# Performance work log

Measured on AMD Instinct MI355X. Metric: run time of the kernel, lower is better.

The kernel has to match this reference:

```python
import jax, jax.numpy as jnp
import numpy as np

# module config (matches init_kwargs)
SLICE_W, SLICE_H = 32, 32
STRIDE, WIDTH_INIT = 8, 8
EMBED_DIM = 512
B, H, W = 64, 32, 4096
PAD = (SLICE_W - WIDTH_INIT) // 2  # 12, width padding with constant value 1.0


def setup_inputs() -> dict:
    key = jax.random.key(0)
    k1, k2, k3, k4, k5 = jax.random.split(key, 5)
    u = lambda k, s: jax.random.uniform(k, s, jnp.float32, -0.08, 0.08)
    return {
        "images": jax.random.normal(k1, (B, 1, H, W), jnp.float32),
        "conv_w": u(k2, (1, 1, 3, 3)),          # Conv2d(1,1,3x3) weight (OIHW)
        "conv_b": u(k3, (1,)),
        "lin_w": u(k4, (SLICE_W * SLICE_H, EMBED_DIM)),  # bridge Linear, stored [in,out]
        "lin_b": u(k5, (EMBED_DIM,)),
    }


def reference(images, conv_w, conv_b, lin_w, lin_b):
    b = images.shape[0]
    # pad width with constant 1 (F.pad(..., 'constant', 1))
    padded = jnp.pad(images, ((0, 0), (0, 0), (0, 0), (PAD, PAD)), constant_values=1.0)
    # vectorized replacement of the python loop over stride positions
    starts = np.arange(0, W - 1, STRIDE)               # [S] static
    S = starts.shape[0]                                # 512
    idx = starts[:, None] + np.arange(SLICE_W)[None, :]  # [S, slice_w]
    sl = padded[:, :, :, idx]                          # [B,1,H,S,slice_w]
    sl = jnp.transpose(sl, (0, 3, 1, 2, 4))            # [B,S,1,H,slice_w]
    x = sl.reshape(b * S, 1, H, SLICE_W)               # pixels
    # embedder: Conv2d(1,1,k=3,pad=1) + ReLU
    y = jax.lax.conv_general_dilated(x, conv_w, (1, 1), ((1, 1), (1, 1)))
    y = jax.nn.relu(y + conv_b[None, :, None, None])
    # bridge: Linear(slice_w*slice_h -> embed_dim)
    flat = y.reshape(b * S, H * SLICE_W)
    out = flat @ lin_w + lin_b
    return out.reshape(b, S, EMBED_DIM)
```

## Files before the change

### kernel.cpp

```cpp
#include <hip/hip_runtime.h>
#include <cstdint>
#include <cstddef>

typedef unsigned short u16;
typedef unsigned int   u32;
typedef __attribute__((ext_vector_type(4))) float  f32x4;
typedef __attribute__((ext_vector_type(8))) __bf16 bf16x8;

#define PSW   1056
#define ASTR  72
#define CFW   4128
#define RPAD  4144

#define WS_BT  0u
#define WS_CF  1048576u
#define WS_AB  (1048576u + 16908288u)
#define WS_NEED (1048576u + 16908288u + 4194304u)

static __device__ __forceinline__ float b2f(u32 u) {
  union { u32 i; float f; } c; c.i = u << 16; return c.f;
}
static __device__ __forceinline__ u16 f2b(float f) {
  union { float f; u32 i; } c; c.f = f;
  return (u16)((c.i + 0x7FFFu + ((c.i >> 16) & 1u)) >> 16);
}

static __device__ __forceinline__ void gl_lds16(const void* g, void* l) {
  __builtin_amdgcn_global_load_lds(
      (__attribute__((address_space(1))) unsigned int*)(void*)g,
      (__attribute__((address_space(3))) unsigned int*)l, 16, 0, 0);
}
static __device__ __forceinline__ void gl_lds4(const void* g, void* l) {
  __builtin_amdgcn_global_load_lds(
      (__attribute__((address_space(1))) unsigned int*)(void*)g,
      (__attribute__((address_space(3))) unsigned int*)l, 4, 0, 0);
}

__global__ __launch_bounds__(256) void transpose_w(const float* __restrict__ lw,
                                                   u16* __restrict__ bt) {
  __shared__ u16 tile[64][65];
  const int t  = threadIdx.x;
  const int c  = t & 63, r0 = t >> 6;
  const int n0 = blockIdx.x * 64;
  const int k0 = blockIdx.y * 64;
#pragma unroll
  for (int rr = 0; rr < 16; ++rr) {
    const int r = r0 * 16 + rr;
    tile[r][c] = f2b(lw[(size_t)(k0 + r) * 512 + n0 + c]);
  }
  __syncthreads();
#pragma unroll
  for (int rr = 0; rr < 16; ++rr) {
    const int r = r0 * 16 + rr;
    bt[(size_t)(n0 + r) * 1024 + k0 + c] = tile[c][r];
  }
}

__global__ __launch_bounds__(256) void prep(
    const float* __restrict__ img, const float* __restrict__ cw,
    const float* __restrict__ cb, u16* __restrict__ cf, u32* __restrict__ ab)
{
  __shared__ __align__(16) float R[3][RPAD];
  const int b = blockIdx.x, h = blockIdx.y, t = threadIdx.x;
  const float* imgb = img + (size_t)b * 32 * 4096;
#pragma unroll
  for (int r = 0; r < 3; ++r) {
    const int hh = h - 1 + r;
    const int live = (hh >= 0 && hh <= 31);
    const float* row = imgb + (ptrdiff_t)hh * 4096;
    for (int k = t; k < 1024; k += 256) {
      f32x4 v = (f32x4)0.0f;
      if (live) v = *(const f32x4*)(row + (k << 2));
      *(f32x4*)(&R[r][12 + (k << 2)]) = v;
    }
    if (t < 12)      R[r][t] = live ? 1.0f : 0.0f;
    else if (t < 24) R[r][4096 + t] = live ? 1.0f : 0.0f;
    else if (t < 48) R[r][4096 + t] = 0.0f;
  }
  __syncthreads();
  float w[9];
#pragma unroll
  for (int q = 0; q < 9; ++q) w[q] = cw[q];
  const float bias = cb[0];
  u16* dst = cf + (size_t)(b * 32 + h) * CFW;
  for (int c = t; c < 258; c += 256) {
    float wf[3][24];
#pragma unroll
    for (int r = 0; r < 3; ++r) {
      const f32x4* Rr = (const f32x4*)&R[r][0];
      f32x4 m = (f32x4)0.0f;
      if (c != 0) m = Rr[4 * c - 1];
      *(f32x4*)&wf[r][0] = m;
#pragma unroll
      for (int u = 1; u < 6; ++u) *(f32x4*)&wf[r][4 * u] = Rr[4 * c - 1 + u];
    }
    float o[16];
#pragma unroll
    for (int j = 0; j < 16; ++j) o[j] = bias;
#pragma unroll
    for (int r = 0; r < 3; ++r) {
      const float w0 = w[r * 3], w1 = w[r * 3 + 1], w2 = w[r * 3 + 2];
#pragma unroll
      for (int j = 0; j < 16; ++j)
        o[j] += w0 * wf[r][j + 3] + w1 * wf[r][j + 4] + w2 * wf[r][j + 5];
    }
    const int xbase = c << 4;
    u32 pk[8];
#pragma unroll
    for (int q = 0; q < 8; ++q) {
      const int x0 = xbase + 2 * q;
      const u32 lo = (x0     < 4120) ? (u32)f2b(fmaxf(o[2 * q],     0.f)) : 0u;
      const u32 hi = (x0 + 1 < 4120) ? (u32)f2b(fmaxf(o[2 * q + 1], 0.f)) : 0u;
      pk[q] = lo | (hi << 16);
    }
    uint4* dp = (uint4*)(dst + xbase);
    dp[0] = make_uint4(pk[0], pk[1], pk[2], pk[3]);
    dp[1] = make_uint4(pk[4], pk[5], pk[6], pk[7]);
  }
  u32* abrow = ab + (size_t)(b * 32 + h) * 512;
#pragma unroll
  for (int ss = 0; ss < 2; ++ss) {
    const int s = t + ss * 256;
    const int X0 = s << 3;
    float o0 = bias, o1 = bias;
#pragma unroll
    for (int r = 0; r < 3; ++r) {
      o0 += w[r * 3 + 1] * R[r][X0]      + w[r * 3 + 2] * R[r][X0 + 1];
      o1 += w[r * 3 + 0] * R[r][X0 + 30] + w[r * 3 + 1] * R[r][X0 + 31];
    }
    abrow[s] = (u32)f2b(fmaxf(o0, 0.f)) | ((u32)f2b(fmaxf(o1, 0.f)) << 16);
  }
}

__global__ __launch_bounds__(256) void gemm_k(
    const u16* __restrict__ cf, const u32* __restrict__ ab,
    const u16* __restrict__ bt, const float* __restrict__ lb,
    float* __restrict__ out)
{
  __shared__ __align__(16) char sm[4224 + 1024 + 16384];
  u16* Ps   = (u16*)sm;
  u32* Ab32 = (u32*)(sm + 4224);
  u16* Bs   = (u16*)(sm + 5248);
  float* Cs = (float*)sm;

  const int t  = threadIdx.x;
  const int nt = blockIdx.x, mt = blockIdx.y;
  const int b  = mt >> 2, s0 = (mt & 3) << 7, n0 = nt << 7;
  const int w  = t >> 6, i = t & 63;
  const int wr = w >> 1, wc = w & 1;
  const int lq = i >> 4, lr = i & 15;

  const int cB = (i & 7) ^ ((i >> 3) & 7);
  const u16* btp = bt + (size_t)(n0 + (w << 5) + (i >> 3)) * 1024 + (cB << 3);
  u16* BsW = Bs + (w << 11);

  const int rP  = (t >= 132) ? 1 : 0;
  const int ccP = t - 132 * rP;
  const u16* cfp  = cf + (size_t)(b * 32 + rP) * CFW + (s0 << 3) + (ccP << 3);
  const u16* cfp2 = cf + (size_t)(b * 32 + 1) * CFW + (s0 << 3) + ((124 + t) << 3);
  u16* PsW = Ps + (w << 9);

  const u32* abp = ab + (size_t)(b * 32 + (t >> 7)) * 512 + s0 + (t & 127);
  u32* AbW = Ab32 + (w << 6);

  f32x4 acc[4][4];
#pragma unroll
  for (int a = 0; a < 4; ++a)
#pragma unroll
    for (int c = 0; c < 4; ++c) acc[a][c] = (f32x4)0.0f;

  for (int kk = 0; kk < 16; ++kk) {
    __syncthreads();
    gl_lds16(btp,              BsW);
    gl_lds16(btp +  8 * 1024,  BsW + 512);
    gl_lds16(btp + 16 * 1024,  BsW + 1024);
    gl_lds16(btp + 24 * 1024,  BsW + 1536);
    gl_lds16(cfp, PsW);
    if (t < 8) gl_lds16(cfp2, Ps + 2048);
    gl_lds4(abp, AbW);
    btp += 64; cfp += 2 * CFW; cfp2 += 2 * CFW; abp += 1024;
    __syncthreads();

#pragma unroll
    for (int kc = 0; kc < 2; ++kc) {
      const int bswz = (((kc << 2) + lq) ^ (lr & 7)) << 3;
      bf16x8 af[4], bfv[4];
#pragma unroll
      for (int im = 0; im < 4; ++im) {
        const int ml = wr * 64 + im * 16 + lr;
        af[im] = __builtin_bit_cast(bf16x8,
            *(const uint4*)(Ps + kc * 1056 + ((ml + lq) << 3)));
        const u32 a32 = Ab32[kc * 128 + ml];
        union { u16 u; __bf16 h; } lo, hi;
        lo.u = (u16)(a32 & 0xffffu); hi.u = (u16)(a32 >> 16);
        if (lq == 0) af[im][0] = lo.h;
        if (lq == 3) af[im][7] = hi.h;
      }
#pragma unroll
      for (int jn = 0; jn < 4; ++jn) {
        const int n = wc * 64 + jn * 16 + lr;
        bfv[jn] = __builtin_bit_cast(bf16x8, *(const uint4*)(Bs + (n << 6) + bswz));
      }
#pragma unroll
      for (int im = 0; im < 4; ++im)
#pragma unroll
        for (int jn = 0; jn < 4; ++jn)
          acc[im][jn] = __builtin_amdgcn_mfma_f32_16x16x32_bf16(
              af[im], bfv[jn], acc[im][jn], 0, 0, 0);
    }
  }

  float lbv[4];
#pragma unroll
  for (int jn = 0; jn < 4; ++jn) lbv[jn] = lb[n0 + wc * 64 + jn * 16 + lr];

  const int erow = t >> 3, ecol = (t & 7) << 4;
  const int grow_base = (mt << 7) + ((erow >> 4) * 64) + (erow & 15);

#pragma unroll
  for (int im = 0; im < 4; ++im) {
    __syncthreads();
#pragma unroll
    for (int jn = 0; jn < 4; ++jn) {
      const int cl = wc * 64 + jn * 16 + lr;
#pragma unroll
      for (int r = 0; r < 4; ++r)
        Cs[(wr * 16 + lq * 4 + r) * 132 + cl] = acc[im][jn][r] + lbv[jn];
    }
    __syncthreads();
    const size_t grow = (size_t)(grow_base + im * 16);
    float* orow = out + grow * 512 + n0 + ecol;
    const float* crow = Cs + erow * 132 + ecol;
#pragma unroll
    for (int p = 0; p < 4; ++p)
      *(f32x4*)(orow + p * 4) = *(const f32x4*)(crow + p * 4);
  }
}

__global__ __launch_bounds__(256) void fused_fallback(
    const float* __restrict__ img, const float* __restrict__ cw,
    const float* __restrict__ cb, const u16* __restrict__ bt,
    const float* __restrict__ lb, float* __restrict__ out)
{
  __shared__ __align__(16) u16 Ps[4 * PSW];
  __shared__ __align__(16) u16 As[128 * ASTR];
  __shared__ __align__(16) u16 Bs[128 * ASTR];
  const int t = threadIdx.x, nt = blockIdx.x, mt = blockIdx.y;
  const int b = mt >> 2, s0 = (mt & 3) << 7, X0 = s0 << 3, n0 = nt << 7;
  const float* imgb = img + (size_t)b * 32 * 4096;
  float cwf[9];
#pragma unroll
  for (int q = 0; q < 9; ++q) cwf[q] = cw[q];
  const float bias = cb[0];
  const int wv = t >> 6, l = t & 63;
  const int wr = wv >> 1, wc = wv & 1, lq = l >> 4, lr = l & 15;
  const int sl = t >> 1, hsel = t & 1;
  f32x4 acc[4][4];
#pragma unroll
  for (int a = 0; a < 4; ++a)
#pragma unroll
    for (int c = 0; c < 4; ++c) acc[a][c] = (f32x4)0.0f;
  for (int kk = 0; kk < 16; ++kk) {
    const int h0 = kk << 1;
    __syncthreads();
    uint4 bsv[4];
#pragma unroll
    for (int p = 0; p < 4; ++p) {
      const int idx8 = t + (p << 8);
      const int n = idx8 >> 3, k8 = idx8 & 7;
      bsv[p] = *(const uint4*)(bt + (size_t)(n0 + n) * 1024 + (kk << 6) + (k8 << 3));
    }
    for (int idx = t; idx < 4 * PSW; idx += 256) {
      const int r = idx / PSW, xi = idx - r * PSW;
      const int h = h0 - 1 + r, x = X0 - 1 + xi;
      u16 v = 0;
      if (h >= 0 && h < 32 && x >= 0 && x < 4120)
        v = (x < 12 || x >= 4108) ? (u16)0x3F80 : f2b(imgb[h * 4096 + (x - 12)]);
      Ps[idx] = v;
    }
    __syncthreads();
    {
      const int pbase = (sl << 3);
#pragma unroll
      for (int wb = 0; wb < 32; wb += 16) {
        float o[16];
#pragma unroll
        for (int j = 0; j < 16; ++j) o[j] = bias;
#pragma unroll
        for (int dr = 0; dr < 3; ++dr) {
          const u16* p = Ps + (hsel + dr) * PSW + pbase + wb;
          const uint4 va = *(const uint4*)p;
          const uint4 vb = *(const uint4*)(p + 8);
          const u32   vc = *(const u32*)(p + 16);
          float win[18];
          win[0] = b2f(va.x & 0xffffu); win[1] = b2f(va.x >> 16);
          win[2] = b2f(va.y & 0xffffu); win[3] = b2f(va.y >> 16);
          win[4] = b2f(va.z & 0xffffu); win[5] = b2f(va.z >> 16);
          win[6] = b2f(va.w & 0xffffu); win[7] = b2f(va.w >> 16);
          win[8] = b2f(vb.x & 0xffffu); win[9] = b2f(vb.x >> 16);
          win[10] = b2f(vb.y & 0xffffu); win[11] = b2f(vb.y >> 16);
          win[12] = b2f(vb.z & 0xffffu); win[13] = b2f(vb.z >> 16);
          win[14] = b2f(vb.w & 0xffffu); win[15] = b2f(vb.w >> 16);
          win[16] = b2f(vc & 0xffffu);   win[17] = b2f(vc >> 16);
          if (wb == 0) win[0] = 0.f; else win[17] = 0.f;
          const float w0 = cwf[dr * 3], w1 = cwf[dr * 3 + 1], w2 = cwf[dr * 3 + 2];
#pragma unroll
          for (int j = 0; j < 16; ++j)
            o[j] += w0 * win[j] + w1 * win[j + 1] + w2 * win[j + 2];
        }
        u32 pk[8];
#pragma unroll
        for (int q = 0; q < 8; ++q)
          pk[q] = (u32)f2b(fmaxf(o[2 * q], 0.f)) | ((u32)f2b(fmaxf(o[2 * q + 1], 0.f)) << 16);
        uint4* dst = (uint4*)(As + sl * ASTR + (hsel << 5) + wb);
        dst[0] = make_uint4(pk[0], pk[1], pk[2], pk[3]);
        dst[1] = make_uint4(pk[4], pk[5], pk[6], pk[7]);
      }
    }
#pragma unroll
    for (int p = 0; p < 4; ++p) {
      const int idx8 = t + (p << 8);
      const int n = idx8 >> 3, k8 = idx8 & 7;
      *(uint4*)(Bs + n * ASTR + (k8 << 3)) = bsv[p];
    }
    __syncthreads();
#pragma unroll
    for (int kc = 0; kc < 2; ++kc) {
      const int ko = (kc << 5) + (lq << 3);
      bf16x8 af[4], bfv[4];
#pragma unroll
      for (int im = 0; im < 4; ++im)
        af[im] = __builtin_bit_cast(bf16x8,
            *(const uint4*)(As + (wr * 64 + im * 16 + lr) * ASTR + ko));
#pragma unroll
      for (int jn = 0; jn < 4; ++jn)
        bfv[jn] = __builtin_bit_cast(bf16x8,
            *(const uint4*)(Bs + (wc * 64 + jn * 16 + lr) * ASTR + ko));
#pragma unroll
      for (int im = 0; im < 4; ++im)
#pragma unroll
        for (int jn = 0; jn < 4; ++jn)
          acc[im][jn] = __builtin_amdgcn_mfma_f32_16x16x32_bf16(
              af[im], bfv[jn], acc[im][jn], 0, 0, 0);
    }
  }
#pragma unroll
  for (int jn = 0; jn < 4; ++jn) {
    const int col = n0 + wc * 64 + jn * 16 + lr;
    const float lbv = lb[col];
#pragma unroll
    for (int im = 0; im < 4; ++im) {
      const int row0 = (mt << 7) + wr * 64 + im * 16 + (lq << 2);
#pragma unroll
      for (int r = 0; r < 4; ++r)
        out[(size_t)(row0 + r) * 512 + col] = acc[im][jn][r] + lbv;
    }
  }
}

extern "C" void kernel_launch(void* const* d_in, const int* in_sizes, int n_in,
                              void* d_out, int out_size, void* d_ws, size_t ws_size,
                              hipStream_t stream) {
  const float* img = (const float*)d_in[0];
  const float* cw  = (const float*)d_in[1];
  const float* cb  = (const float*)d_in[2];
  const float* lw  = (const float*)d_in[3];
  const float* lb  = (const float*)d_in[4];
  float* out = (float*)d_out;

  u16* btw = (u16*)((char*)d_ws + WS_BT);
  transpose_w<<<dim3(8, 16), 256, 0, stream>>>(lw, btw);

  if (ws_size >= WS_NEED) {
    u16* cf = (u16*)((char*)d_ws + WS_CF);
    u32* ab = (u32*)((char*)d_ws + WS_AB);
    prep<<<dim3(64, 32), 256, 0, stream>>>(img, cw, cb, cf, ab);
    gemm_k<<<dim3(4, 256), 256, 0, stream>>>(cf, ab, btw, lb, out);
  } else {
    fused_fallback<<<dim3(4, 256), 256, 0, stream>>>(img, cw, cb, btw, lb, out);
  }
}
```

Measured before the change: 170.3 us.

## Fold weight transpose into prep kernel, rebalance conv work, swizzle GEMM block order

The separate transpose_w launch is merged into prep as an extra row of blocks, which removes one kernel launch and its serialization gap. The conv prep loop now gives each thread 4 outputs over 1030 iterations instead of 16 outputs over 258, so threads are busier and use fewer registers. The padded LDS row is realigned to 16-float offsets so the vector loads stay aligned. The GEMM block index is remapped to group blocks for better L2 locality; the transpose blocks also add some imbalance to prep.

Measured after the change: 165.2 us. 3.0% less time.

```diff
diff --git a/kernel.cpp b/kernel.cpp
--- a/kernel.cpp
+++ b/kernel.cpp
@@ -5,12 +5,13 @@
 typedef unsigned short u16;
 typedef unsigned int   u32;
 typedef __attribute__((ext_vector_type(4))) float  f32x4;
+typedef __attribute__((ext_vector_type(2))) u32    u32x2;
 typedef __attribute__((ext_vector_type(8))) __bf16 bf16x8;
 
 #define PSW   1056
 #define ASTR  72
 #define CFW   4128
-#define RPAD  4144
+#define RPAD  4128
 
 #define WS_BT  0u
 #define WS_CF  1048576u
@@ -58,24 +59,52 @@
 
 __global__ __launch_bounds__(256) void prep(
     const float* __restrict__ img, const float* __restrict__ cw,
-    const float* __restrict__ cb, u16* __restrict__ cf, u32* __restrict__ ab)
+    const float* __restrict__ cb, u16* __restrict__ cf, u32* __restrict__ ab,
+    const float* __restrict__ lw, u16* __restrict__ bt)
 {
   __shared__ __align__(16) float R[3][RPAD];
-  const int b = blockIdx.x, h = blockIdx.y, t = threadIdx.x;
+  const int t = threadIdx.x;
+
+  if (blockIdx.y == 32) {
+    u16* tile = (u16*)&R[0][0];
+    const int c = t & 63, r0 = t >> 6;
+#pragma unroll
+    for (int q = 0; q < 2; ++q) {
+      const int T  = blockIdx.x * 2 + q;
+      const int n0 = (T & 7) << 6, k0 = (T >> 3) << 6;
+      __syncthreads();
+#pragma unroll
+      for (int rr = 0; rr < 16; ++rr) {
+        const int r = r0 * 16 + rr;
+        tile[r * 65 + c] = f2b(lw[(size_t)(k0 + r) * 512 + n0 + c]);
+      }
+      __syncthreads();
+#pragma unroll
+      for (int rr = 0; rr < 16; ++rr) {
+        const int r = r0 * 16 + rr;
+        bt[(size_t)(n0 + r) * 1024 + k0 + c] = tile[c * 65 + r];
+      }
+    }
+    return;
+  }
+
+  const int b = blockIdx.x, h = blockIdx.y;
   const float* imgb = img + (size_t)b * 32 * 4096;
 #pragma unroll
   for (int r = 0; r < 3; ++r) {
     const int hh = h - 1 + r;
     const int live = (hh >= 0 && hh <= 31);
+    const float live1 = live ? 1.0f : 0.0f;
     const float* row = imgb + (ptrdiff_t)hh * 4096;
     for (int k = t; k < 1024; k += 256) {
       f32x4 v = (f32x4)0.0f;
       if (live) v = *(const f32x4*)(row + (k << 2));
-      *(f32x4*)(&R[r][12 + (k << 2)]) = v;
-    }
-    if (t < 12)      R[r][t] = live ? 1.0f : 0.0f;
-    else if (t < 24) R[r][4096 + t] = live ? 1.0f : 0.0f;
-    else if (t < 48) R[r][4096 + t] = 0.0f;
+      *(f32x4*)(&R[r][16 + (k << 2)]) = v;
+    }
+    if (t < 12)      R[r][4 + t]    = live1;
+    else if (t < 24) R[r][4100 + t] = live1;
+    else if (t < 28) R[r][4100 + t] = 0.0f;
+    else if (t < 32) R[r][t - 28]   = 0.0f;
   }
   __syncthreads();
   float w[9];
@@ -83,45 +112,38 @@
   for (int q = 0; q < 9; ++q) w[q] = cw[q];
   const float bias = cb[0];
   u16* dst = cf + (size_t)(b * 32 + h) * CFW;
-  for (int c = t; c < 258; c += 256) {
-    float wf[3][24];
+  if (t == 0) *(uint4*)(dst + 4120) = make_uint4(0u, 0u, 0u, 0u);
+
+  for (int c4 = t; c4 < 1030; c4 += 256) {
+    float wf[3][12];
 #pragma unroll
     for (int r = 0; r < 3; ++r) {
       const f32x4* Rr = (const f32x4*)&R[r][0];
-      f32x4 m = (f32x4)0.0f;
-      if (c != 0) m = Rr[4 * c - 1];
-      *(f32x4*)&wf[r][0] = m;
-#pragma unroll
-      for (int u = 1; u < 6; ++u) *(f32x4*)&wf[r][4 * u] = Rr[4 * c - 1 + u];
-    }
-    float o[16];
-#pragma unroll
-    for (int j = 0; j < 16; ++j) o[j] = bias;
+      *(f32x4*)&wf[r][0] = Rr[c4];
+      *(f32x4*)&wf[r][4] = Rr[c4 + 1];
+      *(f32x4*)&wf[r][8] = Rr[c4 + 2];
+    }
+    float o[4];
+#pragma unroll
+    for (int j = 0; j < 4; ++j) o[j] = bias;
 #pragma unroll
     for (int r = 0; r < 3; ++r) {
       const float w0 = w[r * 3], w1 = w[r * 3 + 1], w2 = w[r * 3 + 2];
 #pragma unroll
-      for (int j = 0; j < 16; ++j)
+      for (int j = 0; j < 4; ++j)
         o[j] += w0 * wf[r][j + 3] + w1 * wf[r][j + 4] + w2 * wf[r][j + 5];
     }
-    const int xbase = c << 4;
-    u32 pk[8];
-#pragma unroll
-    for (int q = 0; q < 8; ++q) {
-      const int x0 = xbase + 2 * q;
-      const u32 lo = (x0     < 4120) ? (u32)f2b(fmaxf(o[2 * q],     0.f)) : 0u;
-      const u32 hi = (x0 + 1 < 4120) ? (u32)f2b(fmaxf(o[2 * q + 1], 0.f)) : 0u;
-      pk[q] = lo | (hi << 16);
-    }
-    uint4* dp = (uint4*)(dst + xbase);
-    dp[0] = make_uint4(pk[0], pk[1], pk[2], pk[3]);
-    dp[1] = make_uint4(pk[4], pk[5], pk[6], pk[7]);
-  }
+    u32x2 pk;
+    pk.x = (u32)f2b(fmaxf(o[0], 0.f)) | ((u32)f2b(fmaxf(o[1], 0.f)) << 16);
+    pk.y = (u32)f2b(fmaxf(o[2], 0.f)) | ((u32)f2b(fmaxf(o[3], 0.f)) << 16);
+    *(u32x2*)(dst + (c4 << 2)) = pk;
+  }
+
   u32* abrow = ab + (size_t)(b * 32 + h) * 512;
 #pragma unroll
   for (int ss = 0; ss < 2; ++ss) {
-    const int s = t + ss * 256;
-    const int X0 = s << 3;
+    const int s  = t + (ss << 8);
+    const int X0 = (s << 3) + 4;
     float o0 = bias, o1 = bias;
 #pragma unroll
     for (int r = 0; r < 3; ++r) {
@@ -144,7 +166,9 @@
   float* Cs = (float*)sm;
 
   const int t  = threadIdx.x;
-  const int nt = blockIdx.x, mt = blockIdx.y;
+  const int orig = blockIdx.y * 4 + blockIdx.x;
+  const int wg   = ((orig & 7) << 7) + (orig >> 3);
+  const int nt = wg & 3, mt = wg >> 2;
   const int b  = mt >> 2, s0 = (mt & 3) << 7, n0 = nt << 7;
   const int w  = t >> 6, i = t & 63;
   const int wr = w >> 1, wc = w & 1;
@@ -369,14 +393,14 @@
   float* out = (float*)d_out;
 
   u16* btw = (u16*)((char*)d_ws + WS_BT);
-  transpose_w<<<dim3(8, 16), 256, 0, stream>>>(lw, btw);
 
   if (ws_size >= WS_NEED) {
-    u16* cf = (u16*)((char*)d_ws + WS_CF);
-    u32* ab = (u32*)((char*)d_ws + WS_AB);
-    prep<<<dim3(64, 32), 256, 0, stream>>>(img, cw, cb, cf, ab);
-    gemm_k<<<dim3(4, 256), 256, 0, stream>>>(cf, ab, btw, lb, out);
+    u16* cfp = (u16*)((char*)d_ws + WS_CF);
+    u32* abp = (u32*)((char*)d_ws + WS_AB);
+    prep<<<dim3(64, 33), 256, 0, stream>>>(img, cw, cb, cfp, abp, lw, btw);
+    gemm_k<<<dim3(4, 256), 256, 0, stream>>>(cfp, abp, btw, lb, out);
   } else {
+    transpose_w<<<dim3(8, 16), 256, 0, stream>>>(lw, btw);
     fused_fallback<<<dim3(4, 256), 256, 0, stream>>>(img, cw, cb, btw, lb, out);
   }
 }
```
